# Kernel optimization log

Measured on AMD Instinct MI355X. Metric: run time of the kernel, lower is better.

## Reference

```python
import jax, jax.numpy as jnp
import numpy as np

P_DIMS = [100, 100, 80, 60, 60]
P = sum(P_DIMS)  # 400
N_STREAMS = len(P_DIMS)
MEM_ITERS = 5
DECAY = 0.8
LR = 0.5        # hebbian_learning_rate
FORGET = 0.9999 # hebbian_forget_rate
NEG_SLOPE = 0.01


def _build_masks():
    idx = np.cumsum([0] + P_DIMS)
    hier = np.zeros((P, P), np.float32)
    for i in range(N_STREAMS):
        for j in range(i, N_STREAMS):
            hier[idx[i]:idx[i + 1], idx[j]:idx[j + 1]] = 1.0
    iters = [MEM_ITERS - f for f in range(N_STREAMS)]  # [5,4,3,2,1]
    rmasks = np.zeros((MEM_ITERS, P), np.float32)
    for it in range(MEM_ITERS):
        for s, r in enumerate(iters):
            if it < r:
                rmasks[it, idx[s]:idx[s + 1]] = 1.0
    return jnp.asarray(hier), jnp.asarray(rmasks)


def setup_inputs() -> dict:
    key = jax.random.key(0)
    k1, k2, k3, k4 = jax.random.split(key, 4)
    B = 512
    return {
        'M_prev': jax.random.normal(k1, (B, P, P), dtype=jnp.float32) * 0.1,
        'p_inferred': jax.random.normal(k2, (B, P), dtype=jnp.float32),
        'p_generated': jax.random.normal(k3, (B, P), dtype=jnp.float32),
        'query': jax.random.normal(k4, (B, P), dtype=jnp.float32),
    }


def reference(M_prev, p_inferred, p_generated, query):
    hier_mask, retrieval_masks = _build_masks()

    # Hebbian update: M = clamp(forget*M_prev + lr*(p-phat)(p+phat)^T, -1, 1) * hier_mask
    outer = (p_inferred - p_generated)[:, :, None] * (p_inferred + p_generated)[:, None, :]
    M = jnp.clip(FORGET * M_prev + LR * outer, -1.0, 1.0) * hier_mask

    # Hierarchical attractor retrieval
    h = jax.nn.leaky_relu(jnp.clip(query, -1.0, 1.0), NEG_SLOPE)

    def step(h, mask):
        mv = jnp.einsum('bpq,bq->bp', M, h)
        upd = jax.nn.leaky_relu(jnp.clip(DECAY * h + mv, -1.0, 1.0), NEG_SLOPE)
        return (1.0 - mask) * h + mask * upd, None

    h, _ = jax.lax.scan(step, h, retrieval_masks)
    return h
```

## Files before the change

### kernel.cpp

```cpp
#include <hip/hip_runtime.h>


#define PDIM 400
#define FORGET 0.9999f
#define LRATE  0.5f
#define DECAY  0.8f
#define SLOPE  0.01f

__device__ __forceinline__ float leaky_clip(float x) {
    x = fminf(fmaxf(x, -1.0f), 1.0f);
    return x > 0.0f ? x : SLOPE * x;
}
__device__ __forceinline__ float clamp1(float x) {
    return fminf(fmaxf(x, -1.0f), 1.0f);
}

__device__ __forceinline__ int c4beg(int p) {
    return (p < 100) ? 0 : (p < 200) ? 25 : (p < 280) ? 50 : (p < 340) ? 70 : 85;
}

__device__ __forceinline__ float wave_sum(float x) {
    x += __int_as_float(__builtin_amdgcn_update_dpp(0, __float_as_int(x), 0xB1,  0xf, 0xf, true));
    x += __int_as_float(__builtin_amdgcn_update_dpp(0, __float_as_int(x), 0x4E,  0xf, 0xf, true));
    x += __int_as_float(__builtin_amdgcn_update_dpp(0, __float_as_int(x), 0x141, 0xf, 0xf, true));
    x += __int_as_float(__builtin_amdgcn_update_dpp(0, __float_as_int(x), 0x140, 0xf, 0xf, true));
    x += __int_as_float(__builtin_amdgcn_update_dpp(0, __float_as_int(x), 0x142, 0xf, 0xf, true));
    x += __int_as_float(__builtin_amdgcn_update_dpp(0, __float_as_int(x), 0x143, 0xf, 0xf, true));
    return __int_as_float(__builtin_amdgcn_readlane(__float_as_int(x), 63));
}

__global__ __launch_bounds__(512, 4)
void hier_mem_kernel(const float* __restrict__ M_prev,
                     const float* __restrict__ p_inf,
                     const float* __restrict__ p_gen,
                     const float* __restrict__ query,
                     float* __restrict__ out)
{
    __shared__ float s_h[2][PDIM];
    __shared__ float s_la[PDIM];

    const int b   = blockIdx.x;
    const int tid = threadIdx.x;
    const int l   = tid & 63;
    const int wid = tid >> 6;
    const float* __restrict__ Mb = M_prev + (size_t)b * PDIM * PDIM;

    if (tid < PDIM) {
        const float pi = p_inf[b * PDIM + tid];
        const float pg = p_gen[b * PDIM + tid];
        s_la[tid]   = LRATE * (pi - pg);
        s_h[0][tid] = leaky_clip(query[b * PDIM + tid]);
    }

    const float4 z4 = make_float4(0.f, 0.f, 0.f, 0.f);
    const float4* __restrict__ pi4 = (const float4*)(p_inf + (size_t)b * PDIM);
    const float4* __restrict__ pg4 = (const float4*)(p_gen + (size_t)b * PDIM);
    float4 bA, bB = z4;
    {
        const float4 x = pi4[l], y = pg4[l];
        bA = make_float4(x.x + y.x, x.y + y.y, x.z + y.z, x.w + y.w);
        if (l < 36) {
            const float4 u = pi4[64 + l], v = pg4[64 + l];
            bB = make_float4(u.x + v.x, u.y + v.y, u.z + v.z, u.w + v.w);
        }
    }
    __syncthreads();

    const int Rt[5] = {400, 340, 280, 200, 100};
    int cur = 0;

    #pragma unroll
    for (int t = 0; t < 5; ++t) {
        const int R = Rt[t];
        const float* __restrict__ hcur = s_h[cur];
        float* __restrict__ hnew = s_h[cur ^ 1];

        float4 hA = *(const float4*)(hcur + 4 * l);
        float4 hB = z4;
        if (l < 36) hB = *(const float4*)(hcur + 256 + 4 * l);

        int p = wid;
        int c4 = 0;
        float4 cA = z4, cB = z4;
        if (p < R) {
            c4 = c4beg(p);
            const float* __restrict__ row = Mb + (size_t)p * PDIM;
            if (l >= c4)               cA = *(const float4*)(row + 4 * l);
            if (l < 36 && 64 + l >= c4) cB = *(const float4*)(row + 256 + 4 * l);
        }
        while (p < R) {
            const int pn = p + 8;
            int c4n = 0;
            float4 nA = z4, nB = z4;
            if (pn < R) {
                c4n = c4beg(pn);
                const float* __restrict__ rn = Mb + (size_t)pn * PDIM;
                if (l >= c4n)                nA = *(const float4*)(rn + 4 * l);
                if (l < 36 && 64 + l >= c4n) nB = *(const float4*)(rn + 256 + 4 * l);
            }

            const float la = s_la[p];
            float acc = 0.f;
            if (l >= c4) {
                float m0 = clamp1(fmaf(FORGET, cA.x, la * bA.x));
                float m1 = clamp1(fmaf(FORGET, cA.y, la * bA.y));
                float m2 = clamp1(fmaf(FORGET, cA.z, la * bA.z));
                float m3 = clamp1(fmaf(FORGET, cA.w, la * bA.w));
                acc = fmaf(m0, hA.x, fmaf(m1, hA.y, fmaf(m2, hA.z, m3 * hA.w)));
            }
            if (l < 36 && 64 + l >= c4) {
                float m0 = clamp1(fmaf(FORGET, cB.x, la * bB.x));
                float m1 = clamp1(fmaf(FORGET, cB.y, la * bB.y));
                float m2 = clamp1(fmaf(FORGET, cB.z, la * bB.z));
                float m3 = clamp1(fmaf(FORGET, cB.w, la * bB.w));
                acc = fmaf(m0, hB.x, fmaf(m1, hB.y, fmaf(m2, hB.z, fmaf(m3, hB.w, acc))));
            }

            const float tot = wave_sum(acc);
            if (l == 0) {
                hnew[p] = leaky_clip(fmaf(DECAY, hcur[p], tot));
            }

            p = pn; c4 = c4n; cA = nA; cB = nB;
        }

        if (tid >= R && tid < PDIM) hnew[tid] = hcur[tid];
        __syncthreads();
        cur ^= 1;
    }

    if (tid < PDIM) {
        out[b * PDIM + tid] = s_h[cur][tid];
    }
}

extern "C" void kernel_launch(void* const* d_in, const int* in_sizes, int n_in,
                              void* d_out, int out_size, void* d_ws, size_t ws_size,
                              hipStream_t stream) {
    const float* M_prev = (const float*)d_in[0];
    const float* p_inf  = (const float*)d_in[1];
    const float* p_gen  = (const float*)d_in[2];
    const float* query  = (const float*)d_in[3];
    float* out = (float*)d_out;

    const int B = in_sizes[1] / PDIM;
    hipLaunchKernelGGL(hier_mem_kernel, dim3(B), dim3(512), 0, stream,
                       M_prev, p_inf, p_gen, query, out);
}
```

Baseline: 494.2 us.

## Cache first 100 rows of updated M in registers across retrieval iterations

Each wave now computes the Hebbian-updated values for its share of the first 100 rows (the stream present in all five iterations) once, and keeps them in register arrays (13 float4 pairs per lane). Later iterations reuse these registers instead of reloading and recomputing those rows from global memory. Rows 100-399 keep the old reload path. Launch bounds drop from 4 to 2 blocks per SM to make room for the larger register footprint, at the cost of occupancy and latency hiding.

```diff
diff --git a/kernel.cpp b/kernel.cpp
--- a/kernel.cpp
+++ b/kernel.cpp
@@ -6,6 +6,7 @@
 #define LRATE  0.5f
 #define DECAY  0.8f
 #define SLOPE  0.01f
+#define MAXJ 13
 
 __device__ __forceinline__ float leaky_clip(float x) {
     x = fminf(fmaxf(x, -1.0f), 1.0f);
@@ -29,12 +30,12 @@
     return __int_as_float(__builtin_amdgcn_readlane(__float_as_int(x), 63));
 }
 
-__global__ __launch_bounds__(512, 4)
-void hier_mem_kernel(const float* __restrict__ M_prev,
-                     const float* __restrict__ p_inf,
-                     const float* __restrict__ p_gen,
-                     const float* __restrict__ query,
-                     float* __restrict__ out)
+__global__ __launch_bounds__(512, 2)
+void hier_mem_v4(const float* __restrict__ M_prev,
+                 const float* __restrict__ p_inf,
+                 const float* __restrict__ p_gen,
+                 const float* __restrict__ query,
+                 float* __restrict__ out)
 {
     __shared__ float s_h[2][PDIM];
     __shared__ float s_la[PDIM];
@@ -66,39 +67,74 @@
     }
     __syncthreads();
 
-    const int Rt[5] = {400, 340, 280, 200, 100};
-    int cur = 0;
-
-    #pragma unroll
-    for (int t = 0; t < 5; ++t) {
-        const int R = Rt[t];
-        const float* __restrict__ hcur = s_h[cur];
-        float* __restrict__ hnew = s_h[cur ^ 1];
-
+    float4 cacheA[MAXJ];
+    float4 cacheB[MAXJ];
+
+    {
+        const float* __restrict__ hcur = s_h[0];
+        float* __restrict__ hnew = s_h[1];
         float4 hA = *(const float4*)(hcur + 4 * l);
         float4 hB = z4;
         if (l < 36) hB = *(const float4*)(hcur + 256 + 4 * l);
 
-        int p = wid;
-        int c4 = 0;
+        float4 pA, pB = z4;
+        {
+            const float* __restrict__ row = Mb + (size_t)wid * PDIM;
+            pA = *(const float4*)(row + 4 * l);
+            if (l < 36) pB = *(const float4*)(row + 256 + 4 * l);
+        }
+        #pragma unroll
+        for (int j = 0; j < MAXJ; ++j) {
+            const int p = wid + 8 * j;
+            if (p < 100) {
+                const int pn = p + 8;
+                float4 nA = z4, nB = z4;
+                if (pn < 100) {
+                    const float* __restrict__ rn = Mb + (size_t)pn * PDIM;
+                    nA = *(const float4*)(rn + 4 * l);
+                    if (l < 36) nB = *(const float4*)(rn + 256 + 4 * l);
+                }
+                const float la = s_la[p];
+                float4 m;
+                m.x = clamp1(fmaf(FORGET, pA.x, la * bA.x));
+                m.y = clamp1(fmaf(FORGET, pA.y, la * bA.y));
+                m.z = clamp1(fmaf(FORGET, pA.z, la * bA.z));
+                m.w = clamp1(fmaf(FORGET, pA.w, la * bA.w));
+                cacheA[j] = m;
+                float acc = fmaf(m.x, hA.x, fmaf(m.y, hA.y, fmaf(m.z, hA.z, m.w * hA.w)));
+                float4 mb;
+                mb.x = clamp1(fmaf(FORGET, pB.x, la * bB.x));
+                mb.y = clamp1(fmaf(FORGET, pB.y, la * bB.y));
+                mb.z = clamp1(fmaf(FORGET, pB.z, la * bB.z));
+                mb.w = clamp1(fmaf(FORGET, pB.w, la * bB.w));
+                cacheB[j] = mb;
+                if (l < 36) {
+                    acc = fmaf(mb.x, hB.x, fmaf(mb.y, hB.y, fmaf(mb.z, hB.z, fmaf(mb.w, hB.w, acc))));
+                }
+                const float tot = wave_sum(acc);
+                if (l == 0) hnew[p] = leaky_clip(fmaf(DECAY, hcur[p], tot));
+                pA = nA; pB = nB;
+            }
+        }
+
+        int p = 100 + wid;
+        int c4 = c4beg(p);
         float4 cA = z4, cB = z4;
-        if (p < R) {
-            c4 = c4beg(p);
+        {
             const float* __restrict__ row = Mb + (size_t)p * PDIM;
-            if (l >= c4)               cA = *(const float4*)(row + 4 * l);
+            if (l >= c4)                cA = *(const float4*)(row + 4 * l);
             if (l < 36 && 64 + l >= c4) cB = *(const float4*)(row + 256 + 4 * l);
         }
-        while (p < R) {
+        while (p < PDIM) {
             const int pn = p + 8;
             int c4n = 0;
             float4 nA = z4, nB = z4;
-            if (pn < R) {
+            if (pn < PDIM) {
                 c4n = c4beg(pn);
                 const float* __restrict__ rn = Mb + (size_t)pn * PDIM;
                 if (l >= c4n)                nA = *(const float4*)(rn + 4 * l);
                 if (l < 36 && 64 + l >= c4n) nB = *(const float4*)(rn + 256 + 4 * l);
             }
-
             const float la = s_la[p];
             float acc = 0.f;
             if (l >= c4) {
@@ -115,13 +151,80 @@
                 float m3 = clamp1(fmaf(FORGET, cB.w, la * bB.w));
                 acc = fmaf(m0, hB.x, fmaf(m1, hB.y, fmaf(m2, hB.z, fmaf(m3, hB.w, acc))));
             }
-
             const float tot = wave_sum(acc);
-            if (l == 0) {
-                hnew[p] = leaky_clip(fmaf(DECAY, hcur[p], tot));
-            }
-
+            if (l == 0) hnew[p] = leaky_clip(fmaf(DECAY, hcur[p], tot));
             p = pn; c4 = c4n; cA = nA; cB = nB;
+        }
+        __syncthreads();
+    }
+
+    const int Rt[5] = {400, 340, 280, 200, 100};
+    int cur = 1;
+
+    #pragma unroll
+    for (int t = 1; t < 5; ++t) {
+        const int R = Rt[t];
+        const float* __restrict__ hcur = s_h[cur];
+        float* __restrict__ hnew = s_h[cur ^ 1];
+
+        float4 hA = *(const float4*)(hcur + 4 * l);
+        float4 hB = z4;
+        if (l < 36) hB = *(const float4*)(hcur + 256 + 4 * l);
+
+        #pragma unroll
+        for (int j = 0; j < MAXJ; ++j) {
+            const int p = wid + 8 * j;
+            if (p < 100) {
+                const float4 m  = cacheA[j];
+                float acc = fmaf(m.x, hA.x, fmaf(m.y, hA.y, fmaf(m.z, hA.z, m.w * hA.w)));
+                if (l < 36) {
+                    const float4 mb = cacheB[j];
+                    acc = fmaf(mb.x, hB.x, fmaf(mb.y, hB.y, fmaf(mb.z, hB.z, fmaf(mb.w, hB.w, acc))));
+                }
+                const float tot = wave_sum(acc);
+                if (l == 0) hnew[p] = leaky_clip(fmaf(DECAY, hcur[p], tot));
+            }
+        }
+
+        int p = 100 + wid;
+        if (p < R) {
+            int c4 = c4beg(p);
+            float4 cA = z4, cB = z4;
+            {
+                const float* __restrict__ row = Mb + (size_t)p * PDIM;
+                if (l >= c4)                cA = *(const float4*)(row + 4 * l);
+                if (l < 36 && 64 + l >= c4) cB = *(const float4*)(row + 256 + 4 * l);
+            }
+            while (p < R) {
+                const int pn = p + 8;
+                int c4n = 0;
+                float4 nA = z4, nB = z4;
+                if (pn < R) {
+                    c4n = c4beg(pn);
+                    const float* __restrict__ rn = Mb + (size_t)pn * PDIM;
+                    if (l >= c4n)                nA = *(const float4*)(rn + 4 * l);
+                    if (l < 36 && 64 + l >= c4n) nB = *(const float4*)(rn + 256 + 4 * l);
+                }
+                const float la = s_la[p];
+                float acc = 0.f;
+                if (l >= c4) {
+                    float m0 = clamp1(fmaf(FORGET, cA.x, la * bA.x));
+                    float m1 = clamp1(fmaf(FORGET, cA.y, la * bA.y));
+                    float m2 = clamp1(fmaf(FORGET, cA.z, la * bA.z));
+                    float m3 = clamp1(fmaf(FORGET, cA.w, la * bA.w));
+                    acc = fmaf(m0, hA.x, fmaf(m1, hA.y, fmaf(m2, hA.z, m3 * hA.w)));
+                }
+                if (l < 36 && 64 + l >= c4) {
+                    float m0 = clamp1(fmaf(FORGET, cB.x, la * bB.x));
+                    float m1 = clamp1(fmaf(FORGET, cB.y, la * bB.y));
+                    float m2 = clamp1(fmaf(FORGET, cB.z, la * bB.z));
+                    float m3 = clamp1(fmaf(FORGET, cB.w, la * bB.w));
+                    acc = fmaf(m0, hB.x, fmaf(m1, hB.y, fmaf(m2, hB.z, fmaf(m3, hB.w, acc))));
+                }
+                const float tot = wave_sum(acc);
+                if (l == 0) hnew[p] = leaky_clip(fmaf(DECAY, hcur[p], tot));
+                p = pn; c4 = c4n; cA = nA; cB = nB;
+            }
         }
 
         if (tid >= R && tid < PDIM) hnew[tid] = hcur[tid];
@@ -129,9 +232,7 @@
         cur ^= 1;
     }
 
-    if (tid < PDIM) {
-        out[b * PDIM + tid] = s_h[cur][tid];
-    }
+    if (tid < PDIM) out[b * PDIM + tid] = s_h[cur][tid];
 }
 
 extern "C" void kernel_launch(void* const* d_in, const int* in_sizes, int n_in,
@@ -144,6 +245,6 @@
     float* out = (float*)d_out;
 
     const int B = in_sizes[1] / PDIM;
-    hipLaunchKernelGGL(hier_mem_kernel, dim3(B), dim3(512), 0, stream,
+    hipLaunchKernelGGL(hier_mem_v4, dim3(B), dim3(512), 0, stream,
                        M_prev, p_inf, p_gen, query, out);
 }
```

After: 522.7 us. 1.06x slower.
